# Performance work log

Hardware: AMD Instinct MI355X
Metric: run time of the kernel (lower is better)

## Reference

```python
import jax, jax.numpy as jnp
import numpy as np

N, E, F_IN, H, C = 169343, 1166243, 128, 128, 40
BN_EPS = 1e-5


def setup_inputs() -> dict:
    key = jax.random.key(0)
    ks = jax.random.split(key, 16)
    inp = {
        "x": jax.random.normal(ks[0], (N, F_IN), jnp.float32),
        "edge_index": jax.random.randint(ks[1], (2, E), 0, N, dtype=jnp.int64),
        "W1": jax.random.normal(ks[2], (F_IN, H), jnp.float32) * (1.0 / np.sqrt(F_IN)),
        "b1": jnp.zeros((H,), jnp.float32),
        "g1": jnp.ones((H,), jnp.float32),
        "be1": jnp.zeros((H,), jnp.float32),
        "m1": jax.random.normal(ks[3], (H,), jnp.float32) * 0.1,
        "v1": jax.random.uniform(ks[4], (H,), jnp.float32, 0.5, 1.5),
        "W2": jax.random.normal(ks[5], (H, H), jnp.float32) * (1.0 / np.sqrt(H)),
        "b2": jnp.zeros((H,), jnp.float32),
        "g2": jnp.ones((H,), jnp.float32),
        "be2": jnp.zeros((H,), jnp.float32),
        "m2": jax.random.normal(ks[6], (H,), jnp.float32) * 0.1,
        "v2": jax.random.uniform(ks[7], (H,), jnp.float32, 0.5, 1.5),
        "W3": jax.random.normal(ks[8], (H, C), jnp.float32) * (1.0 / np.sqrt(H)),
        "b3": jnp.zeros((C,), jnp.float32),
    }
    return inp


def _gcn_conv(h, W, b, src, dst, norm, n_nodes):
    # GCNConv: out = D^-1/2 (A+I) D^-1/2 (h W) + b
    hw = h @ W                                   # [N, H] dense GEMM
    msgs = hw[src] * norm[:, None]               # [E', H] gather (irregular)
    agg = jax.ops.segment_sum(msgs, dst, num_segments=n_nodes)  # scatter-add
    return agg + b


def _bn_eval(h, gamma, beta, mean, var):
    return (h - mean) * jax.lax.rsqrt(var + BN_EPS) * gamma + beta


def reference(x, edge_index, W1, b1, g1, be1, m1, v1,
              W2, b2, g2, be2, m2, v2, W3, b3):
    n = x.shape[0]
    loops = jnp.arange(n, dtype=edge_index.dtype)
    src = jnp.concatenate([edge_index[0], loops])  # add self-loops
    dst = jnp.concatenate([edge_index[1], loops])
    deg = jax.ops.segment_sum(jnp.ones_like(dst, dtype=x.dtype), dst, num_segments=n)
    dinv = jax.lax.rsqrt(jnp.maximum(deg, 1.0))
    norm = dinv[src] * dinv[dst]                  # [E+N]

    # layer stack (eval mode: dropout is identity, repeated ReLU idempotent)
    h = jax.nn.relu(_gcn_conv(x, W1, b1, src, dst, norm, n))
    h = jax.nn.relu(_bn_eval(h, g1, be1, m1, v1))
    h = jax.nn.relu(_gcn_conv(h, W2, b2, src, dst, norm, n))
    h = jax.nn.relu(_bn_eval(h, g2, be2, m2, v2))
    out = h @ W3 + b3                              # final Linear [N, C]
    return jax.nn.log_softmax(out, axis=-1), jnp.var(out, ddof=1)
```

## Files before the change

kernel.cpp:

```cpp
#include <hip/hip_runtime.h>
#include <math.h>

#define BN_EPS 1e-5f

typedef _Float16 f16;
typedef __attribute__((ext_vector_type(4))) _Float16 f16x4;
typedef __attribute__((ext_vector_type(8))) _Float16 f16x8;
typedef __attribute__((ext_vector_type(4))) float f32x4;

__device__ __forceinline__ int edge_at(const void* ei, long long idx, int is64) {
    if (is64) return (int)((const long long*)ei)[idx];
    return ((const int*)ei)[idx];
}

__global__ void init_kernel(const void* ei, int* flag, int* deg_i,
                            double* scal, int n) {
    int i = blockIdx.x * 256 + threadIdx.x;
    if (i < n) deg_i[i] = 0;
    if (blockIdx.x == 0 && threadIdx.x == 0) {
        scal[0] = 0.0; scal[1] = 0.0;
        const int* p = (const int*)ei;
        int f = 1;
        for (int k = 0; k < 64; k++)
            if (p[2 * k + 1] != 0) { f = 0; break; }
        *flag = f;
    }
}

__global__ void degi_kernel(const void* ei, const int* flag, int* deg_i, int E) {
    int e = blockIdx.x * 256 + threadIdx.x;
    if (e >= E) return;
    int is64 = *flag;
    int d = edge_at(ei, (long long)E + e, is64);
    atomicAdd(&deg_i[d], 1);
}

__global__ __launch_bounds__(256) void scan1_kernel(
    const int* __restrict__ in, int* __restrict__ excl, int* bsum, int n) {
    __shared__ int sh[256];
    const int tid = threadIdx.x;
    const int base = blockIdx.x * 2048 + tid * 8;
    int v[8];
    #pragma unroll
    for (int i = 0; i < 8; i++) v[i] = (base + i < n) ? in[base + i] : 0;
    int tsum = 0;
    #pragma unroll
    for (int i = 0; i < 8; i++) { int t = v[i]; v[i] = tsum; tsum += t; }
    sh[tid] = tsum;
    __syncthreads();
    for (int off = 1; off < 256; off <<= 1) {
        int t = 0;
        if (tid >= off) t = sh[tid - off];
        __syncthreads();
        if (tid >= off) sh[tid] += t;
        __syncthreads();
    }
    int texcl = sh[tid] - tsum;
    #pragma unroll
    for (int i = 0; i < 8; i++)
        if (base + i < n) excl[base + i] = texcl + v[i];
    if (tid == 255 && bsum) bsum[blockIdx.x] = sh[255];
}

__global__ void scan3_kernel(int* rowptr, const int* __restrict__ boff,
                             int* cursor, const int* __restrict__ deg_i,
                             float* __restrict__ dinv, int n, int E) {
    int i = blockIdx.x * 256 + threadIdx.x;
    if (i < n) {
        int val = rowptr[i] + boff[i >> 11];
        rowptr[i] = val;
        cursor[i] = val;
        dinv[i] = rsqrtf((float)(deg_i[i] + 1));
    }
    if (i == 0) rowptr[n] = E;
}

__global__ void fill_kernel(const void* ei, const int* flag,
                            int* cursor, int* col, int E) {
    int e = blockIdx.x * 256 + threadIdx.x;
    if (e >= E) return;
    int is64 = *flag;
    int s = edge_at(ei, e, is64);
    int d = edge_at(ei, (long long)E + e, is64);
    int pos = atomicAdd(&cursor[d], 1);
    col[pos] = s;
}

__global__ __launch_bounds__(256) void prep_w_kernel(
    const float* __restrict__ W, f16* __restrict__ Wth, f16* __restrict__ Wtl) {
    for (int f = blockIdx.x * 256 + threadIdx.x; f < 128 * 128;
         f += gridDim.x * 256) {
        int k = f >> 7, nn = f & 127;
        float wv = W[f];
        f16 h = (f16)wv;
        f16 l = (f16)(wv - (float)h);
        Wth[nn * 128 + k] = h;
        Wtl[nn * 128 + k] = l;
    }
}

#define APAD 40
__global__ __launch_bounds__(256) void gemm_l1_kernel(
    const float* __restrict__ X, const f16* __restrict__ Wth,
    const f16* __restrict__ Wtl, const float* __restrict__ dinv,
    f16* __restrict__ out, int M) {
    __shared__ f16 Ah[128 * APAD];
    __shared__ f16 Bh[128 * APAD];
    __shared__ f16 Bl[128 * APAD];
    const int t = threadIdx.x;
    const int r0 = blockIdx.x * 128;
    const int w = t >> 6, lane = t & 63;
    const int m0 = (w >> 1) * 64, n0 = (w & 1) * 64;
    const int fr = lane & 15;
    const int kb = (lane >> 4) * 8;

    f32x4 acc[4][4];
    #pragma unroll
    for (int i = 0; i < 4; i++)
        #pragma unroll
        for (int j = 0; j < 4; j++) acc[i][j] = (f32x4)0.f;

    for (int k0 = 0; k0 < 128; k0 += 32) {
        #pragma unroll
        for (int i = 0; i < 4; i++) {
            int f = t + i * 256;
            int row = f >> 3, kq = (f & 7) * 4;
            float4 v = make_float4(0.f, 0.f, 0.f, 0.f);
            if (r0 + row < M)
                v = *(const float4*)&X[(size_t)(r0 + row) * 128 + k0 + kq];
            *(f16x4*)&Ah[row * APAD + kq] =
                (f16x4){(f16)v.x, (f16)v.y, (f16)v.z, (f16)v.w};
        }
        #pragma unroll
        for (int i = 0; i < 2; i++) {
            int f = t + i * 256;
            int nrow = f >> 2, kq = (f & 3) * 8;
            int gb = nrow * 128 + k0 + kq;
            int lb = nrow * APAD + kq;
            *(uint4*)&Bh[lb] = *(const uint4*)&Wth[gb];
            *(uint4*)&Bl[lb] = *(const uint4*)&Wtl[gb];
        }
        __syncthreads();

        f16x8 a0[4], b0[4], xx[4];
        #pragma unroll
        for (int i = 0; i < 4; i++) {
            a0[i] = *(const f16x8*)&Ah[(m0 + i * 16 + fr) * APAD + kb];
            b0[i] = *(const f16x8*)&Bh[(n0 + i * 16 + fr) * APAD + kb];
        }
        #pragma unroll
        for (int i = 0; i < 4; i++)
            #pragma unroll
            for (int j = 0; j < 4; j++)
                acc[i][j] = __builtin_amdgcn_mfma_f32_16x16x32_f16(
                    a0[i], b0[j], acc[i][j], 0, 0, 0);
        #pragma unroll
        for (int i = 0; i < 4; i++)
            xx[i] = *(const f16x8*)&Bl[(n0 + i * 16 + fr) * APAD + kb];
        #pragma unroll
        for (int i = 0; i < 4; i++)
            #pragma unroll
            for (int j = 0; j < 4; j++)
                acc[i][j] = __builtin_amdgcn_mfma_f32_16x16x32_f16(
                    a0[i], xx[j], acc[i][j], 0, 0, 0);
        __syncthreads();
    }

    #pragma unroll
    for (int i = 0; i < 4; i++) {
        #pragma unroll
        for (int r = 0; r < 4; r++) {
            int row = r0 + m0 + i * 16 + (lane >> 4) * 4 + r;
            if (row < M) {
                float di = dinv[row];
                #pragma unroll
                for (int j = 0; j < 4; j++)
                    out[(size_t)row * 128 + n0 + j * 16 + fr] =
                        (f16)(acc[i][j][r] * di);
            }
        }
    }
}

__global__ __launch_bounds__(256) void gemm_l2_kernel(
    const f16* __restrict__ X, const f16* __restrict__ Wth,
    const f16* __restrict__ Wtl, const float* __restrict__ dinv,
    f16* __restrict__ out, int M) {
    __shared__ f16 Ax[128 * APAD];
    __shared__ f16 Bh[128 * APAD];
    __shared__ f16 Bl[128 * APAD];
    const int t = threadIdx.x;
    const int r0 = blockIdx.x * 128;
    const int w = t >> 6, lane = t & 63;
    const int m0 = (w >> 1) * 64, n0 = (w & 1) * 64;
    const int fr = lane & 15;
    const int kb = (lane >> 4) * 8;

    f32x4 acc[4][4];
    #pragma unroll
    for (int i = 0; i < 4; i++)
        #pragma unroll
        for (int j = 0; j < 4; j++) acc[i][j] = (f32x4)0.f;

    for (int k0 = 0; k0 < 128; k0 += 32) {
        #pragma unroll
        for (int i = 0; i < 2; i++) {
            int f = t + i * 256;
            int row = f >> 2, kq = (f & 3) * 8;
            uint4 v = make_uint4(0u, 0u, 0u, 0u);
            if (r0 + row < M)
                v = *(const uint4*)&X[(size_t)(r0 + row) * 128 + k0 + kq];
            *(uint4*)&Ax[row * APAD + kq] = v;
        }
        #pragma unroll
        for (int i = 0; i < 2; i++) {
            int f = t + i * 256;
            int nrow = f >> 2, kq = (f & 3) * 8;
            int gb = nrow * 128 + k0 + kq;
            int lb = nrow * APAD + kq;
            *(uint4*)&Bh[lb] = *(const uint4*)&Wth[gb];
            *(uint4*)&Bl[lb] = *(const uint4*)&Wtl[gb];
        }
        __syncthreads();

        f16x8 a0[4], b0[4], xx[4];
        #pragma unroll
        for (int i = 0; i < 4; i++) {
            a0[i] = *(const f16x8*)&Ax[(m0 + i * 16 + fr) * APAD + kb];
            b0[i] = *(const f16x8*)&Bh[(n0 + i * 16 + fr) * APAD + kb];
        }
        #pragma unroll
        for (int i = 0; i < 4; i++)
            #pragma unroll
            for (int j = 0; j < 4; j++)
                acc[i][j] = __builtin_amdgcn_mfma_f32_16x16x32_f16(
                    a0[i], b0[j], acc[i][j], 0, 0, 0);
        #pragma unroll
        for (int i = 0; i < 4; i++)
            xx[i] = *(const f16x8*)&Bl[(n0 + i * 16 + fr) * APAD + kb];
        #pragma unroll
        for (int i = 0; i < 4; i++)
            #pragma unroll
            for (int j = 0; j < 4; j++)
                acc[i][j] = __builtin_amdgcn_mfma_f32_16x16x32_f16(
                    a0[i], xx[j], acc[i][j], 0, 0, 0);
        __syncthreads();
    }

    #pragma unroll
    for (int i = 0; i < 4; i++) {
        #pragma unroll
        for (int r = 0; r < 4; r++) {
            int row = r0 + m0 + i * 16 + (lane >> 4) * 4 + r;
            if (row < M) {
                float di = dinv[row];
                #pragma unroll
                for (int j = 0; j < 4; j++)
                    out[(size_t)row * 128 + n0 + j * 16 + fr] =
                        (f16)(acc[i][j][r] * di);
            }
        }
    }
}

__global__ __launch_bounds__(256) void agg_kernel(
    const f16* __restrict__ hs, const int* __restrict__ rowptr,
    const int* __restrict__ col, const float* __restrict__ dinv,
    const float* __restrict__ b, const float* __restrict__ g,
    const float* __restrict__ be, const float* __restrict__ m,
    const float* __restrict__ v, f16* __restrict__ h, int M) {
    const int node = blockIdx.x * 8 + (threadIdx.x >> 5);
    if (node >= M) return;
    const int lane = threadIdx.x & 31;
    const int c = lane * 4;
    const f16* __restrict__ base = hs + c;

    f16x4 sv = *(const f16x4*)&base[(size_t)node * 128];
    float a0[4] = {(float)sv[0], (float)sv[1], (float)sv[2], (float)sv[3]};
    float a1[4] = {0.f, 0.f, 0.f, 0.f};
    float a2[4] = {0.f, 0.f, 0.f, 0.f};
    float a3[4] = {0.f, 0.f, 0.f, 0.f};
    const int beg = rowptr[node], end = rowptr[node + 1];
    int j = beg;
    for (; j + 3 < end; j += 4) {
        int s0 = col[j], s1 = col[j + 1], s2 = col[j + 2], s3 = col[j + 3];
        f16x4 v0 = *(const f16x4*)&base[(size_t)s0 * 128];
        f16x4 v1 = *(const f16x4*)&base[(size_t)s1 * 128];
        f16x4 v2 = *(const f16x4*)&base[(size_t)s2 * 128];
        f16x4 v3 = *(const f16x4*)&base[(size_t)s3 * 128];
        #pragma unroll
        for (int q = 0; q < 4; q++) {
            a0[q] += (float)v0[q]; a1[q] += (float)v1[q];
            a2[q] += (float)v2[q]; a3[q] += (float)v3[q];
        }
    }
    if (j + 1 < end) {
        int s0 = col[j], s1 = col[j + 1];
        f16x4 v0 = *(const f16x4*)&base[(size_t)s0 * 128];
        f16x4 v1 = *(const f16x4*)&base[(size_t)s1 * 128];
        #pragma unroll
        for (int q = 0; q < 4; q++) { a0[q] += (float)v0[q]; a1[q] += (float)v1[q]; }
        j += 2;
    }
    if (j < end) {
        int s0 = col[j];
        f16x4 v0 = *(const f16x4*)&base[(size_t)s0 * 128];
        #pragma unroll
        for (int q = 0; q < 4; q++) a0[q] += (float)v0[q];
    }
    const float di = dinv[node];
    f16x4 r;
    #pragma unroll
    for (int q = 0; q < 4; q++) {
        int cc = c + q;
        float s = (a0[q] + a1[q]) + (a2[q] + a3[q]);
        float tt = fmaxf(di * s + b[cc], 0.f);
        tt = (tt - m[cc]) * (g[cc] * rsqrtf(v[cc] + BN_EPS)) + be[cc];
        r[q] = (f16)fmaxf(tt, 0.f);
    }
    *(f16x4*)&h[(size_t)node * 128 + c] = r;
}

__global__ __launch_bounds__(256) void gemm_out_kernel(
    const f16* __restrict__ H, const float* __restrict__ W3,
    const float* __restrict__ b3, float* __restrict__ out,
    double* __restrict__ scal, int M) {
    __shared__ float Hs[256][20];
    __shared__ float Ws[128][40];
    const int t  = threadIdx.x;
    const int r0 = blockIdx.x * 256;
    #pragma unroll
    for (int i = 0; i < 5; i++) {
        int f = t + i * 256;
        ((float4*)Ws)[f] = ((const float4*)W3)[f];
    }
    const int rg = t >> 2;
    const int cb = (t & 3) * 10;
    float acc[4][10];
    #pragma unroll
    for (int i = 0; i < 4; i++)
        #pragma unroll
        for (int j = 0; j < 10; j++) acc[i][j] = 0.f;

    for (int k0 = 0; k0 < 128; k0 += 16) {
        __syncthreads();
        #pragma unroll
        for (int i = 0; i < 4; i++) {
            int f = t + i * 256;
            int r = f >> 2, c4 = (f & 3) * 4;
            float4 hv = make_float4(0.f, 0.f, 0.f, 0.f);
            if (r0 + r < M) {
                f16x4 hx = *(const f16x4*)&H[(size_t)(r0 + r) * 128 + k0 + c4];
                hv = make_float4((float)hx[0], (float)hx[1],
                                 (float)hx[2], (float)hx[3]);
            }
            *(float4*)&Hs[r][c4] = hv;
        }
        __syncthreads();
        #pragma unroll
        for (int k4 = 0; k4 < 4; k4++) {
            float hv[4][4];
            #pragma unroll
            for (int i = 0; i < 4; i++) {
                float4 h4 = *(const float4*)&Hs[rg + 64 * i][k4 * 4];
                hv[i][0] = h4.x; hv[i][1] = h4.y; hv[i][2] = h4.z; hv[i][3] = h4.w;
            }
            #pragma unroll
            for (int q = 0; q < 4; q++) {
                int k = k0 + k4 * 4 + q;
                float wv[10];
                #pragma unroll
                for (int j = 0; j < 5; j++) {
                    float2 w2 = *(const float2*)&Ws[k][cb + 2 * j];
                    wv[2 * j] = w2.x; wv[2 * j + 1] = w2.y;
                }
                #pragma unroll
                for (int i = 0; i < 4; i++)
                    #pragma unroll
                    for (int j = 0; j < 10; j++)
                        acc[i][j] = fmaf(hv[i][q], wv[j], acc[i][j]);
            }
        }
    }

    float s1 = 0.f, s2 = 0.f;
    #pragma unroll
    for (int i = 0; i < 4; i++) {
        int row = r0 + rg + 64 * i;
        float vb[10];
        #pragma unroll
        for (int j = 0; j < 10; j++) vb[j] = acc[i][j] + b3[cb + j];
        float mx = vb[0];
        #pragma unroll
        for (int j = 1; j < 10; j++) mx = fmaxf(mx, vb[j]);
        mx = fmaxf(mx, __shfl_xor(mx, 1));
        mx = fmaxf(mx, __shfl_xor(mx, 2));
        float se = 0.f;
        #pragma unroll
        for (int j = 0; j < 10; j++) se += expf(vb[j] - mx);
        se += __shfl_xor(se, 1);
        se += __shfl_xor(se, 2);
        float ls = mx + logf(se);
        if (row < M) {
            #pragma unroll
            for (int j = 0; j < 10; j++) {
                out[(size_t)row * 40 + cb + j] = vb[j] - ls;
                s1 += vb[j];
                s2 += vb[j] * vb[j];
            }
        }
    }
    #pragma unroll
    for (int o = 32; o; o >>= 1) { s1 += __shfl_xor(s1, o); s2 += __shfl_xor(s2, o); }
    __shared__ double sh1[4], sh2[4];
    if ((t & 63) == 0) { sh1[t >> 6] = (double)s1; sh2[t >> 6] = (double)s2; }
    __syncthreads();
    if (t == 0) {
        atomicAdd(&scal[0], sh1[0] + sh1[1] + sh1[2] + sh1[3]);
        atomicAdd(&scal[1], sh2[0] + sh2[1] + sh2[2] + sh2[3]);
    }
}

__global__ void var_kernel(const double* scal, float* out, long long nn, long long off) {
    double s1 = scal[0], s2 = scal[1];
    out[off] = (float)((s2 - s1 * s1 / (double)nn) / (double)(nn - 1));
}

extern "C" void kernel_launch(void* const* d_in, const int* in_sizes, int n_in,
                              void* d_out, int out_size, void* d_ws, size_t ws_size,
                              hipStream_t stream) {
    const float* x   = (const float*)d_in[0];
    const void*  ei  = d_in[1];
    const float* W1  = (const float*)d_in[2];
    const float* b1  = (const float*)d_in[3];
    const float* g1  = (const float*)d_in[4];
    const float* be1 = (const float*)d_in[5];
    const float* m1  = (const float*)d_in[6];
    const float* v1  = (const float*)d_in[7];
    const float* W2  = (const float*)d_in[8];
    const float* b2  = (const float*)d_in[9];
    const float* g2  = (const float*)d_in[10];
    const float* be2 = (const float*)d_in[11];
    const float* m2  = (const float*)d_in[12];
    const float* v2  = (const float*)d_in[13];
    const float* W3  = (const float*)d_in[14];
    const float* b3  = (const float*)d_in[15];

    const int n = in_sizes[0] / 128;
    const int E = in_sizes[1] / 2;
    float* out = (float*)d_out;

    size_t nh   = (size_t)n * 128;
    size_t npad = ((size_t)n + 3) & ~(size_t)3;
    size_t Epad = ((size_t)E + 3) & ~(size_t)3;
    double* scal   = (double*)d_ws;
    f16*    A      = (f16*)(scal + 2);
    f16*    B      = A + nh;
    float*  dinv   = (float*)(B + nh);
    int*    deg_i  = (int*)(dinv + npad);
    int*    rowptr = deg_i + npad;
    int*    cursor = rowptr + npad + 4;
    int*    bsum   = cursor + npad;
    int*    boff   = bsum + 128;
    int*    flag   = boff + 128;
    int*    col    = flag + 4;
    f16*    Wt1h   = (f16*)(col + Epad);
    f16*    Wt1l   = Wt1h + 128 * 128;
    f16*    Wt2h   = Wt1l + 128 * 128;
    f16*    Wt2l   = Wt2h + 128 * 128;

    const int nb_n   = (n + 255) / 256;
    const int nb_e   = (E + 255) / 256;
    const int nb_gm  = (n + 127) / 128;
    const int nb_agg = (n + 7) / 8;
    const int nb_g3  = (n + 255) / 256;
    const int nb_sc  = (n + 2047) / 2048;

    init_kernel<<<nb_n, 256, 0, stream>>>(ei, flag, deg_i, scal, n);
    degi_kernel<<<nb_e, 256, 0, stream>>>(ei, flag, deg_i, E);
    prep_w_kernel<<<64, 256, 0, stream>>>(W1, Wt1h, Wt1l);
    prep_w_kernel<<<64, 256, 0, stream>>>(W2, Wt2h, Wt2l);

    scan1_kernel<<<nb_sc, 256, 0, stream>>>(deg_i, rowptr, bsum, n);
    scan1_kernel<<<1, 256, 0, stream>>>(bsum, boff, nullptr, nb_sc);
    scan3_kernel<<<nb_n, 256, 0, stream>>>(rowptr, boff, cursor, deg_i, dinv, n, E);
    fill_kernel<<<nb_e, 256, 0, stream>>>(ei, flag, cursor, col, E);

    gemm_l1_kernel<<<nb_gm, 256, 0, stream>>>(x, Wt1h, Wt1l, dinv, A, n);
    agg_kernel<<<nb_agg, 256, 0, stream>>>(A, rowptr, col, dinv,
                                           b1, g1, be1, m1, v1, B, n);
    gemm_l2_kernel<<<nb_gm, 256, 0, stream>>>(B, Wt2h, Wt2l, dinv, A, n);
    agg_kernel<<<nb_agg, 256, 0, stream>>>(A, rowptr, col, dinv,
                                           b2, g2, be2, m2, v2, B, n);
    gemm_out_kernel<<<nb_g3, 256, 0, stream>>>(B, W3, b3, out, scal, n);
    var_kernel<<<1, 1, 0, stream>>>(scal, out, (long long)n * 40, (long long)n * 40);
}
```

Before: 565.5 us.

## Reuse degree-atomic ranks for CSR fill, split aggregation across half-waves, fuse small kernels

The degree-counting atomics now record each edge's rank, so the CSR fill writes col[rowptr[d]+rank[e]] directly instead of doing a second atomic pass on a cursor array. The aggregation kernel gives each node a full 64-lane wave, with two half-waves handling alternating neighbours and combining through a shuffle, which gives more parallelism per node at the cost of idle lanes on low-degree nodes. The two weight-prep launches become one, and the variance kernel is folded into the last block of the output GEMM through a done-counter, which removes launches. Storing the ranks costs an extra E-sized int buffer write and read.

Measured after the change: 579.9 us. 2.5% more time.

```diff
diff --git a/kernel.cpp b/kernel.cpp
--- a/kernel.cpp
+++ b/kernel.cpp
@@ -14,11 +14,12 @@
 }
 
 __global__ void init_kernel(const void* ei, int* flag, int* deg_i,
-                            double* scal, int n) {
+                            double* scal, int* done, int n) {
     int i = blockIdx.x * 256 + threadIdx.x;
     if (i < n) deg_i[i] = 0;
     if (blockIdx.x == 0 && threadIdx.x == 0) {
         scal[0] = 0.0; scal[1] = 0.0;
+        *done = 0;
         const int* p = (const int*)ei;
         int f = 1;
         for (int k = 0; k < 64; k++)
@@ -27,12 +28,13 @@
     }
 }
 
-__global__ void degi_kernel(const void* ei, const int* flag, int* deg_i, int E) {
+__global__ void degi_kernel(const void* ei, const int* flag, int* deg_i,
+                            int* __restrict__ rank, int E) {
     int e = blockIdx.x * 256 + threadIdx.x;
     if (e >= E) return;
     int is64 = *flag;
     int d = edge_at(ei, (long long)E + e, is64);
-    atomicAdd(&deg_i[d], 1);
+    rank[e] = atomicAdd(&deg_i[d], 1);
 }
 
 __global__ __launch_bounds__(256) void scan1_kernel(
@@ -63,39 +65,42 @@
 }
 
 __global__ void scan3_kernel(int* rowptr, const int* __restrict__ boff,
-                             int* cursor, const int* __restrict__ deg_i,
+                             const int* __restrict__ deg_i,
                              float* __restrict__ dinv, int n, int E) {
     int i = blockIdx.x * 256 + threadIdx.x;
     if (i < n) {
-        int val = rowptr[i] + boff[i >> 11];
-        rowptr[i] = val;
-        cursor[i] = val;
+        rowptr[i] = rowptr[i] + boff[i >> 11];
         dinv[i] = rsqrtf((float)(deg_i[i] + 1));
     }
     if (i == 0) rowptr[n] = E;
 }
 
 __global__ void fill_kernel(const void* ei, const int* flag,
-                            int* cursor, int* col, int E) {
+                            const int* __restrict__ rowptr,
+                            const int* __restrict__ rank,
+                            int* __restrict__ col, int E) {
     int e = blockIdx.x * 256 + threadIdx.x;
     if (e >= E) return;
     int is64 = *flag;
     int s = edge_at(ei, e, is64);
     int d = edge_at(ei, (long long)E + e, is64);
-    int pos = atomicAdd(&cursor[d], 1);
-    col[pos] = s;
+    col[rowptr[d] + rank[e]] = s;
 }
 
 __global__ __launch_bounds__(256) void prep_w_kernel(
-    const float* __restrict__ W, f16* __restrict__ Wth, f16* __restrict__ Wtl) {
-    for (int f = blockIdx.x * 256 + threadIdx.x; f < 128 * 128;
+    const float* __restrict__ W1, f16* __restrict__ Wt1h, f16* __restrict__ Wt1l,
+    const float* __restrict__ W2, f16* __restrict__ Wt2h, f16* __restrict__ Wt2l) {
+    for (int f = blockIdx.x * 256 + threadIdx.x; f < 2 * 128 * 128;
          f += gridDim.x * 256) {
-        int k = f >> 7, nn = f & 127;
-        float wv = W[f];
+        int which = f >> 14, g = f & 16383;
+        int k = g >> 7, nn = g & 127;
+        const float* W = which ? W2 : W1;
+        f16* Wh = which ? Wt2h : Wt1h;
+        f16* Wl = which ? Wt2l : Wt1l;
+        float wv = W[g];
         f16 h = (f16)wv;
-        f16 l = (f16)(wv - (float)h);
-        Wth[nn * 128 + k] = h;
-        Wtl[nn * 128 + k] = l;
+        Wh[nn * 128 + k] = h;
+        Wl[nn * 128 + k] = (f16)(wv - (float)h);
     }
 }
 
@@ -269,38 +274,28 @@
     const float* __restrict__ b, const float* __restrict__ g,
     const float* __restrict__ be, const float* __restrict__ m,
     const float* __restrict__ v, f16* __restrict__ h, int M) {
-    const int node = blockIdx.x * 8 + (threadIdx.x >> 5);
+    const int node = blockIdx.x * 4 + (threadIdx.x >> 6);
     if (node >= M) return;
-    const int lane = threadIdx.x & 31;
-    const int c = lane * 4;
+    const int lane = threadIdx.x & 63;
+    const int half = lane >> 5;
+    const int c = (lane & 31) * 4;
     const f16* __restrict__ base = hs + c;
 
-    f16x4 sv = *(const f16x4*)&base[(size_t)node * 128];
-    float a0[4] = {(float)sv[0], (float)sv[1], (float)sv[2], (float)sv[3]};
+    float a0[4] = {0.f, 0.f, 0.f, 0.f};
     float a1[4] = {0.f, 0.f, 0.f, 0.f};
-    float a2[4] = {0.f, 0.f, 0.f, 0.f};
-    float a3[4] = {0.f, 0.f, 0.f, 0.f};
+    if (half == 0) {
+        f16x4 sv = *(const f16x4*)&base[(size_t)node * 128];
+        #pragma unroll
+        for (int q = 0; q < 4; q++) a0[q] = (float)sv[q];
+    }
     const int beg = rowptr[node], end = rowptr[node + 1];
-    int j = beg;
-    for (; j + 3 < end; j += 4) {
-        int s0 = col[j], s1 = col[j + 1], s2 = col[j + 2], s3 = col[j + 3];
+    int j = beg + half;
+    for (; j + 2 < end; j += 4) {
+        int s0 = col[j], s1 = col[j + 2];
         f16x4 v0 = *(const f16x4*)&base[(size_t)s0 * 128];
         f16x4 v1 = *(const f16x4*)&base[(size_t)s1 * 128];
-        f16x4 v2 = *(const f16x4*)&base[(size_t)s2 * 128];
-        f16x4 v3 = *(const f16x4*)&base[(size_t)s3 * 128];
-        #pragma unroll
-        for (int q = 0; q < 4; q++) {
-            a0[q] += (float)v0[q]; a1[q] += (float)v1[q];
-            a2[q] += (float)v2[q]; a3[q] += (float)v3[q];
-        }
-    }
-    if (j + 1 < end) {
-        int s0 = col[j], s1 = col[j + 1];
-        f16x4 v0 = *(const f16x4*)&base[(size_t)s0 * 128];
-        f16x4 v1 = *(const f16x4*)&base[(size_t)s1 * 128];
         #pragma unroll
         for (int q = 0; q < 4; q++) { a0[q] += (float)v0[q]; a1[q] += (float)v1[q]; }
-        j += 2;
     }
     if (j < end) {
         int s0 = col[j];
@@ -312,19 +307,21 @@
     f16x4 r;
     #pragma unroll
     for (int q = 0; q < 4; q++) {
+        float s = a0[q] + a1[q];
+        s += __shfl_xor(s, 32);
         int cc = c + q;
-        float s = (a0[q] + a1[q]) + (a2[q] + a3[q]);
         float tt = fmaxf(di * s + b[cc], 0.f);
         tt = (tt - m[cc]) * (g[cc] * rsqrtf(v[cc] + BN_EPS)) + be[cc];
         r[q] = (f16)fmaxf(tt, 0.f);
     }
-    *(f16x4*)&h[(size_t)node * 128 + c] = r;
+    if (half == 0)
+        *(f16x4*)&h[(size_t)node * 128 + c] = r;
 }
 
 __global__ __launch_bounds__(256) void gemm_out_kernel(
     const f16* __restrict__ H, const float* __restrict__ W3,
     const float* __restrict__ b3, float* __restrict__ out,
-    double* __restrict__ scal, int M) {
+    double* __restrict__ scal, int* __restrict__ done, int M) {
     __shared__ float Hs[256][20];
     __shared__ float Ws[128][40];
     const int t  = threadIdx.x;
@@ -418,12 +415,16 @@
     if (t == 0) {
         atomicAdd(&scal[0], sh1[0] + sh1[1] + sh1[2] + sh1[3]);
         atomicAdd(&scal[1], sh2[0] + sh2[1] + sh2[2] + sh2[3]);
-    }
-}
-
-__global__ void var_kernel(const double* scal, float* out, long long nn, long long off) {
-    double s1 = scal[0], s2 = scal[1];
-    out[off] = (float)((s2 - s1 * s1 / (double)nn) / (double)(nn - 1));
+        __threadfence();
+        int prev = atomicAdd(done, 1);
+        if (prev == (int)gridDim.x - 1) {
+            __threadfence();
+            double t1 = atomicAdd(&scal[0], 0.0);
+            double t2 = atomicAdd(&scal[1], 0.0);
+            long long nn = (long long)M * 40;
+            out[nn] = (float)((t2 - t1 * t1 / (double)nn) / (double)(nn - 1));
+        }
+    }
 }
 
 extern "C" void kernel_launch(void* const* d_in, const int* in_sizes, int n_in,
@@ -459,11 +460,12 @@
     float*  dinv   = (float*)(B + nh);
     int*    deg_i  = (int*)(dinv + npad);
     int*    rowptr = deg_i + npad;
-    int*    cursor = rowptr + npad + 4;
-    int*    bsum   = cursor + npad;
+    int*    rank   = rowptr + npad + 4;
+    int*    bsum   = rank + Epad;
     int*    boff   = bsum + 128;
     int*    flag   = boff + 128;
-    int*    col    = flag + 4;
+    int*    done   = flag + 4;
+    int*    col    = done + 4;
     f16*    Wt1h   = (f16*)(col + Epad);
     f16*    Wt1l   = Wt1h + 128 * 128;
     f16*    Wt2h   = Wt1l + 128 * 128;
@@ -472,19 +474,18 @@
     const int nb_n   = (n + 255) / 256;
     const int nb_e   = (E + 255) / 256;
     const int nb_gm  = (n + 127) / 128;
-    const int nb_agg = (n + 7) / 8;
+    const int nb_agg = (n + 3) / 4;
     const int nb_g3  = (n + 255) / 256;
     const int nb_sc  = (n + 2047) / 2048;
 
-    init_kernel<<<nb_n, 256, 0, stream>>>(ei, flag, deg_i, scal, n);
-    degi_kernel<<<nb_e, 256, 0, stream>>>(ei, flag, deg_i, E);
-    prep_w_kernel<<<64, 256, 0, stream>>>(W1, Wt1h, Wt1l);
-    prep_w_kernel<<<64, 256, 0, stream>>>(W2, Wt2h, Wt2l);
+    init_kernel<<<nb_n, 256, 0, stream>>>(ei, flag, deg_i, scal, done, n);
+    degi_kernel<<<nb_e, 256, 0, stream>>>(ei, flag, deg_i, rank, E);
+    prep_w_kernel<<<128, 256, 0, stream>>>(W1, Wt1h, Wt1l, W2, Wt2h, Wt2l);
 
     scan1_kernel<<<nb_sc, 256, 0, stream>>>(deg_i, rowptr, bsum, n);
     scan1_kernel<<<1, 256, 0, stream>>>(bsum, boff, nullptr, nb_sc);
-    scan3_kernel<<<nb_n, 256, 0, stream>>>(rowptr, boff, cursor, deg_i, dinv, n, E);
-    fill_kernel<<<nb_e, 256, 0, stream>>>(ei, flag, cursor, col, E);
+    scan3_kernel<<<nb_n, 256, 0, stream>>>(rowptr, boff, deg_i, dinv, n, E);
+    fill_kernel<<<nb_e, 256, 0, stream>>>(ei, flag, rowptr, rank, col, E);
 
     gemm_l1_kernel<<<nb_gm, 256, 0, stream>>>(x, Wt1h, Wt1l, dinv, A, n);
     agg_kernel<<<nb_agg, 256, 0, stream>>>(A, rowptr, col, dinv,
@@ -492,6 +493,5 @@
     gemm_l2_kernel<<<nb_gm, 256, 0, stream>>>(B, Wt2h, Wt2l, dinv, A, n);
     agg_kernel<<<nb_agg, 256, 0, stream>>>(A, rowptr, col, dinv,
                                            b2, g2, be2, m2, v2, B, n);
-    gemm_out_kernel<<<nb_g3, 256, 0, stream>>>(B, W3, b3, out, scal, n);
-    var_kernel<<<1, 1, 0, stream>>>(scal, out, (long long)n * 40, (long long)n * 40);
-}
+    gemm_out_kernel<<<nb_g3, 256, 0, stream>>>(B, W3, b3, out, scal, done, n);
+}
```
